# Kernel optimization log

Hardware: AMD Instinct MI355X
Metric: run time of the kernel (lower is better)

The kernel has to match this reference:

```python
import jax, jax.numpy as jnp
import numpy as np

N = 8192  # dimension; degree = 2


def setup_inputs() -> dict:
    key = jax.random.key(0)
    k1, k2 = jax.random.split(key)
    num_coeffs = N + N * (N - 1) // 2  # sum_{k=1..2} C(N,k)
    return {
        "input": jax.random.normal(k1, (N,), dtype=jnp.float32),
        "coeffs": jax.random.normal(k2, (num_coeffs,), dtype=jnp.float32),
    }


def reference(input, coeffs):
    # Hamiltonian polynomial: sum over all 1- and 2-subsets of variables,
    # terms ordered [deg-1 terms (lex), deg-2 terms (lex)] to match
    # torch.combinations concatenation order, then dotted with coeffs.
    n = input.shape[0]
    # np.triu_indices(k=1) enumerates (i,j) with i<j in row-major (lex) order,
    # exactly matching torch.combinations(x, r=2).
    iu0, iu1 = np.triu_indices(n, k=1)
    terms1 = input                      # [n]
    terms2 = input[iu0] * input[iu1]    # [C(n,2)] pairwise products
    terms = jnp.concatenate([terms1, terms2])
    return terms @ coeffs
```

## Files before the change

kernel.cpp:

```cpp
#include <hip/hip_runtime.h>
#include <cstdint>

#define N 8192
#define BLK 256
#define NBLOCKS 4096

__device__ __forceinline__ float row_partial(const float* __restrict__ c2,
                                             const float* __restrict__ x,
                                             long long O, int L, int i) {
    const int t = threadIdx.x;
    const float* cp = c2 + O;
    const float* xp = x + i + 1;
    float s = 0.0f;

    int pro = (int)((4 - (O & 3)) & 3);
    if (pro > L) pro = L;
    if (t < pro) s += cp[t] * xp[t];

    const int R = L - pro;
    const int V = R >> 2;
    const int tail = R & 3;

    const float4* __restrict__ cv = (const float4*)(cp + pro);
    const float*  __restrict__ xv = xp + pro;
    for (int v = t; v < V; v += BLK) {
        float4 c = cv[v];
        const int e = v << 2;
        s += c.x * xv[e] + c.y * xv[e + 1] + c.z * xv[e + 2] + c.w * xv[e + 3];
    }
    if (t < tail) {
        const int e = (V << 2) + t;
        s += cp[pro + e] * xv[e];
    }
    return s;
}

__global__ __launch_bounds__(BLK) void ham_main(const float* __restrict__ x,
                                                const float* __restrict__ coeffs,
                                                float* __restrict__ ws) {
    const int b = blockIdx.x;
    const int t = threadIdx.x;
    const float* __restrict__ c1 = coeffs;
    const float* __restrict__ c2 = coeffs + N;

    float acc = 0.0f;

    {
        const int i1 = b;
        const long long O1 = (long long)i1 * (2LL * N - i1 - 1) / 2;
        const int L1 = N - 1 - i1;
        const float s1 = row_partial(c2, x, O1, L1, i1);
        acc += x[i1] * s1;
    }
    {
        const int i2 = N - 2 - b;
        if (i2 > b) {
            const long long O2 = (long long)i2 * (2LL * N - i2 - 1) / 2;
            const int L2 = N - 1 - i2;
            const float s2 = row_partial(c2, x, O2, L2, i2);
            acc += x[i2] * s2;
        }
    }

    {
        const int g = b * BLK + t;
        if (g < N) acc += c1[g] * x[g];
    }

    #pragma unroll
    for (int o = 32; o > 0; o >>= 1) acc += __shfl_down(acc, o, 64);
    __shared__ float smem[BLK / 64];
    const int wave = t >> 6;
    const int lane = t & 63;
    if (lane == 0) smem[wave] = acc;
    __syncthreads();
    if (t == 0) {
        float v = 0.0f;
        #pragma unroll
        for (int w = 0; w < BLK / 64; ++w) v += smem[w];
        ws[b] = v;
    }
}

__global__ __launch_bounds__(1024) void ham_reduce(const float* __restrict__ ws,
                                                   float* __restrict__ out) {
    const int t = threadIdx.x;
    float v = 0.0f;
    for (int idx = t; idx < NBLOCKS; idx += 1024) v += ws[idx];
    #pragma unroll
    for (int o = 32; o > 0; o >>= 1) v += __shfl_down(v, o, 64);
    __shared__ float smem[16];
    const int wave = t >> 6;
    const int lane = t & 63;
    if (lane == 0) smem[wave] = v;
    __syncthreads();
    if (t == 0) {
        float s = 0.0f;
        #pragma unroll
        for (int w = 0; w < 16; ++w) s += smem[w];
        out[0] = s;
    }
}

extern "C" void kernel_launch(void* const* d_in, const int* in_sizes, int n_in,
                              void* d_out, int out_size, void* d_ws, size_t ws_size,
                              hipStream_t stream) {
    const float* x      = (const float*)d_in[0];
    const float* coeffs = (const float*)d_in[1];
    float* out = (float*)d_out;
    float* ws  = (float*)d_ws;

    ham_main<<<NBLOCKS, BLK, 0, stream>>>(x, coeffs, ws);
    ham_reduce<<<1, 1024, 0, stream>>>(ws, out);
}
```

Measured before the change: 197.6 us.

## Stage x in de-interleaved shared memory and process four row pairs per block

Each block loads the whole input vector into LDS, split into four residue-class arrays, so the x operands of the coefficient dot products come from LDS instead of unaligned global loads. The grid shrinks to 1024 blocks of 512 threads, each handling four balanced row pairs, and the final reduction reads the 1024 partials with one float4 per thread. This is meant to cut global load instructions and per-block overhead, at the cost of 32 KB of LDS per block and an extra staging phase that limits occupancy.

```diff
diff --git a/kernel.cpp b/kernel.cpp
--- a/kernel.cpp
+++ b/kernel.cpp
@@ -2,35 +2,44 @@
 #include <cstdint>
 
 #define N 8192
-#define BLK 256
-#define NBLOCKS 4096
+#define BLK 512
+#define NBLK 1024
+#define NPAIRS 4096
 
 __device__ __forceinline__ float row_partial(const float* __restrict__ c2,
-                                             const float* __restrict__ x,
-                                             long long O, int L, int i) {
+                                             const float (&xs)[4][2048],
+                                             int O, int L, int i) {
     const int t = threadIdx.x;
     const float* cp = c2 + O;
-    const float* xp = x + i + 1;
+    const int xb0 = i + 1;
     float s = 0.0f;
 
-    int pro = (int)((4 - (O & 3)) & 3);
+    int pro = (4 - (O & 3)) & 3;
     if (pro > L) pro = L;
-    if (t < pro) s += cp[t] * xp[t];
+    if (t < pro) {
+        const int xi = xb0 + t;
+        s += cp[t] * xs[xi & 3][xi >> 2];
+    }
 
     const int R = L - pro;
     const int V = R >> 2;
     const int tail = R & 3;
+    const float4* __restrict__ cv = (const float4*)(cp + pro);
+    const int xb = xb0 + pro;
 
-    const float4* __restrict__ cv = (const float4*)(cp + pro);
-    const float*  __restrict__ xv = xp + pro;
     for (int v = t; v < V; v += BLK) {
-        float4 c = cv[v];
-        const int e = v << 2;
-        s += c.x * xv[e] + c.y * xv[e + 1] + c.z * xv[e + 2] + c.w * xv[e + 3];
+        const float4 c = cv[v];
+        const int xi = xb + (v << 2);
+        const float x0 = xs[xi & 3][xi >> 2];
+        const float x1 = xs[(xi + 1) & 3][(xi + 1) >> 2];
+        const float x2 = xs[(xi + 2) & 3][(xi + 2) >> 2];
+        const float x3 = xs[(xi + 3) & 3][(xi + 3) >> 2];
+        s += c.x * x0 + c.y * x1 + c.z * x2 + c.w * x3;
     }
     if (t < tail) {
         const int e = (V << 2) + t;
-        s += cp[pro + e] * xv[e];
+        const int xi = xb + e;
+        s += cp[pro + e] * xs[xi & 3][xi >> 2];
     }
     return s;
 }
@@ -38,33 +47,40 @@
 __global__ __launch_bounds__(BLK) void ham_main(const float* __restrict__ x,
                                                 const float* __restrict__ coeffs,
                                                 float* __restrict__ ws) {
+    __shared__ float xs[4][2048];
+    const int t = threadIdx.x;
     const int b = blockIdx.x;
-    const int t = threadIdx.x;
     const float* __restrict__ c1 = coeffs;
     const float* __restrict__ c2 = coeffs + N;
 
+    {
+        const float4* __restrict__ x4 = (const float4*)x;
+        for (int k = t; k < 2048; k += BLK) {
+            const float4 v = x4[k];
+            xs[0][k] = v.x; xs[1][k] = v.y; xs[2][k] = v.z; xs[3][k] = v.w;
+        }
+    }
+    __syncthreads();
+
     float acc = 0.0f;
 
-    {
-        const int i1 = b;
-        const long long O1 = (long long)i1 * (2LL * N - i1 - 1) / 2;
-        const int L1 = N - 1 - i1;
-        const float s1 = row_partial(c2, x, O1, L1, i1);
-        acc += x[i1] * s1;
-    }
-    {
-        const int i2 = N - 2 - b;
-        if (i2 > b) {
-            const long long O2 = (long long)i2 * (2LL * N - i2 - 1) / 2;
-            const int L2 = N - 1 - i2;
-            const float s2 = row_partial(c2, x, O2, L2, i2);
-            acc += x[i2] * s2;
+    #pragma unroll
+    for (int pp = 0; pp < 4; ++pp) {
+        const int p = b + pp * NBLK;
+        const int i1 = p;
+        const int O1 = (i1 * (2 * N - i1 - 1)) >> 1;
+        acc += xs[i1 & 3][i1 >> 2] * row_partial(c2, xs, O1, N - 1 - i1, i1);
+
+        const int i2 = N - 2 - p;
+        if (i2 > i1) {
+            const int O2 = (i2 * (2 * N - i2 - 1)) >> 1;
+            acc += xs[i2 & 3][i2 >> 2] * row_partial(c2, xs, O2, N - 1 - i2, i2);
         }
     }
 
-    {
-        const int g = b * BLK + t;
-        if (g < N) acc += c1[g] * x[g];
+    if (t < 8) {
+        const int g = (b << 3) + t;
+        acc += c1[g] * xs[g & 3][g >> 2];
     }
 
     #pragma unroll
@@ -82,24 +98,20 @@
     }
 }
 
-__global__ __launch_bounds__(1024) void ham_reduce(const float* __restrict__ ws,
-                                                   float* __restrict__ out) {
+__global__ __launch_bounds__(256) void ham_reduce(const float* __restrict__ ws,
+                                                  float* __restrict__ out) {
     const int t = threadIdx.x;
-    float v = 0.0f;
-    for (int idx = t; idx < NBLOCKS; idx += 1024) v += ws[idx];
+    const float4* __restrict__ w4 = (const float4*)ws;
+    const float4 v4 = w4[t];
+    float v = v4.x + v4.y + v4.z + v4.w;
     #pragma unroll
     for (int o = 32; o > 0; o >>= 1) v += __shfl_down(v, o, 64);
-    __shared__ float smem[16];
+    __shared__ float smem[4];
     const int wave = t >> 6;
     const int lane = t & 63;
     if (lane == 0) smem[wave] = v;
     __syncthreads();
-    if (t == 0) {
-        float s = 0.0f;
-        #pragma unroll
-        for (int w = 0; w < 16; ++w) s += smem[w];
-        out[0] = s;
-    }
+    if (t == 0) out[0] = smem[0] + smem[1] + smem[2] + smem[3];
 }
 
 extern "C" void kernel_launch(void* const* d_in, const int* in_sizes, int n_in,
@@ -110,6 +122,6 @@
     float* out = (float*)d_out;
     float* ws  = (float*)d_ws;
 
-    ham_main<<<NBLOCKS, BLK, 0, stream>>>(x, coeffs, ws);
-    ham_reduce<<<1, 1024, 0, stream>>>(ws, out);
+    ham_main<<<NBLK, BLK, 0, stream>>>(x, coeffs, ws);
+    ham_reduce<<<1, 256, 0, stream>>>(ws, out);
 }
```

Result: no change. 201.1 us (+1.8%).
